# Optimization experiments

Hardware: AMD Instinct MI355X
Metric: run time of the kernel (lower is better)

The kernel has to match this reference:

```python
import jax, jax.numpy as jnp
import numpy as np

B, L, P = 16, 768, 256
EPS = 1e-6


def setup_inputs() -> dict:
    key = jax.random.key(0)
    k1, k2, k3, k4, k5 = jax.random.split(key, 5)
    pred = jax.random.normal(k1, (B, L, 3), dtype=jnp.float32) * 5.0
    target = pred + 0.5 * jax.random.normal(k2, (B, L, 3), dtype=jnp.float32)
    gen_mask = jax.random.randint(k3, (B, L), 0, 2).astype(jnp.int32)
    poc = jax.random.normal(k4, (B, P, 3), dtype=jnp.float32) * 5.0
    poc_mask = jax.random.randint(k5, (B, P), 0, 2).astype(jnp.int32)
    return {"pred": pred, "target": target, "gen_mask": gen_mask, "poc": poc, "poc_mask": poc_mask}


def _extract(fea, gm):
    # pad_sequence([fea[i][gm[i].bool()]]) equivalent, padded to L (extra zero
    # rows beyond the batch-max length are fully masked downstream, so losses
    # are identical to torch's pad-to-max behavior).
    order = jnp.argsort(jnp.where(gm > 0, 0, 1), axis=1)  # stable: valid rows first
    idx = order[..., None] if fea.ndim == 3 else order
    g = jnp.take_along_axis(fea, idx, axis=1)
    keep = jnp.arange(fea.shape[1])[None, :] < gm.sum(axis=1)[:, None]
    k = keep[..., None] if fea.ndim == 3 else keep
    return g * k.astype(fea.dtype)


def _masked_mean(t, m):
    # t: [B, L', 2]  m: [B, L']
    valid = jnp.clip(m.sum(axis=-1), 1e-6, None)
    return jnp.mean((t * m[..., None]).sum(axis=(-1, -2)) / valid)


def _cdist(a, b):
    # Gram-trick pairwise distances; [B, La, Lb] only (no [B,La,Lb,3] blowup).
    sq = (jnp.sum(a * a, -1)[:, :, None] + jnp.sum(b * b, -1)[:, None, :]
          - 2.0 * jnp.einsum('bid,bjd->bij', a, b))
    return jnp.sqrt(jnp.maximum(sq, 1e-12))


def _ca_angles(c):
    v1 = c[:, :-2] - c[:, 1:-1]
    v2 = c[:, 2:] - c[:, 1:-1]
    cos = jnp.sum(v1 * v2, -1) / (jnp.linalg.norm(v1, axis=-1) * jnp.linalg.norm(v2, axis=-1) + EPS)
    return jnp.arccos(jnp.clip(cos, -1.0, 1.0))


def _dihedrals(c):
    p0, p1, p2, p3 = c[:, :-3], c[:, 1:-2], c[:, 2:-1], c[:, 3:]
    v1, v2, v3 = p1 - p0, p2 - p1, p3 - p2
    n1 = jnp.cross(v1, v2)
    n2 = jnp.cross(v2, v3)
    cos = jnp.sum(n1 * n2, -1) / (jnp.linalg.norm(n1, axis=-1) * jnp.linalg.norm(n2, axis=-1) + EPS)
    phi = jnp.arccos(jnp.clip(cos, -1.0, 1.0))
    sign = jnp.sign(jnp.sum(jnp.cross(n1, n2) * v2, -1))
    return sign * phi


def _sincos(a):
    return jnp.stack([jnp.sin(a), jnp.cos(a)], axis=-1)


def _loss(pred, target, gen_mask, poc, poc_mask):
    gm = gen_mask.astype(jnp.float32)
    pred_e = _extract(pred, gen_mask)
    target_e = _extract(target, gen_mask)
    mask = _extract(gm, gen_mask)

    angle_loss = _masked_mean((_sincos(_ca_angles(pred_e)) - _sincos(_ca_angles(target_e))) ** 2,
                              mask[:, 1:-1])
    torsion_loss = _masked_mean((_sincos(_dihedrals(pred_e)) - _sincos(_dihedrals(target_e))) ** 2,
                                mask[:, 2:-1])

    d1 = _cdist(pred_e, pred_e)
    d2 = _cdist(target_e, target_e)
    dmask = mask[:, :, None] * mask[:, None, :]
    denom = jnp.sum(dmask, axis=(-1, -2)) + 1e-8
    dist_loss = jnp.mean(jnp.sum((d1 - d2) ** 2 * dmask, axis=(-1, -2)) / denom)
    clash = jnp.where((d1 < 3.8) & (d1 > 2.0), (3.8 - d1) ** 2, 0.0)
    clash_loss = jnp.mean(jnp.sum(clash * dmask, axis=(-1, -2)) / denom)

    # poc branch: source computes inter distances but then overwrites with
    # mean(dist_loss); replicated faithfully (inter_dist_loss == dist_loss).
    _ = _cdist(pred_e, poc)
    _ = _cdist(target_e, poc)
    inter_dist_loss = dist_loss

    return jnp.stack([angle_loss, torsion_loss, dist_loss, inter_dist_loss, clash_loss])


def reference(pred, target, gen_mask, poc, poc_mask):
    return _loss(pred, target, gen_mask, poc, poc_mask)
```

## Files before the change

### kernel.cpp

```cpp
#include <hip/hip_runtime.h>
#include <math.h>

#define BATCH 16
#define LSEQ 768
#define NCHUNK 16
#define NBLK (NCHUNK*BATCH)
#define NT 768
#define NWAVE (NT/64)


__device__ inline void angle_sc4(const float4* __restrict__ c, int i, float& s, float& co) {
    float4 a = c[i], b = c[i+1], d = c[i+2];
    float v1x = a.x-b.x, v1y = a.y-b.y, v1z = a.z-b.z;
    float v2x = d.x-b.x, v2y = d.y-b.y, v2z = d.z-b.z;
    float dot = v1x*v2x + v1y*v2y + v1z*v2z;
    float n1 = sqrtf(v1x*v1x + v1y*v1y + v1z*v1z);
    float n2 = sqrtf(v2x*v2x + v2y*v2y + v2z*v2z);
    float cv = dot / (n1*n2 + 1e-6f);
    cv = fminf(1.f, fmaxf(-1.f, cv));
    co = cv;
    s  = sqrtf(fmaxf(0.f, 1.f - cv*cv));
}

__device__ inline void dih_sc4(const float4* __restrict__ c, int i, float& s, float& co) {
    float4 p0 = c[i], p1 = c[i+1], p2 = c[i+2], p3 = c[i+3];
    float v1x = p1.x-p0.x, v1y = p1.y-p0.y, v1z = p1.z-p0.z;
    float v2x = p2.x-p1.x, v2y = p2.y-p1.y, v2z = p2.z-p1.z;
    float v3x = p3.x-p2.x, v3y = p3.y-p2.y, v3z = p3.z-p2.z;
    float n1x = v1y*v2z - v1z*v2y, n1y = v1z*v2x - v1x*v2z, n1z = v1x*v2y - v1y*v2x;
    float n2x = v2y*v3z - v2z*v3y, n2y = v2z*v3x - v2x*v3z, n2z = v2x*v3y - v2y*v3x;
    float dot = n1x*n2x + n1y*n2y + n1z*n2z;
    float l1 = sqrtf(n1x*n1x + n1y*n1y + n1z*n1z);
    float l2 = sqrtf(n2x*n2x + n2y*n2y + n2z*n2z);
    float cv = dot / (l1*l2 + 1e-6f);
    cv = fminf(1.f, fmaxf(-1.f, cv));
    float sinp = sqrtf(fmaxf(0.f, 1.f - cv*cv));
    float cx = n1y*n2z - n1z*n2y, cy = n1z*n2x - n1x*n2z, cz = n1x*n2y - n1y*n2x;
    float sg = cx*v2x + cy*v2y + cz*v2z;
    float sgn = (sg > 0.f) ? 1.f : ((sg < 0.f) ? -1.f : 0.f);
    co = cv;
    s  = sgn * sinp;
}


__global__ __launch_bounds__(NT) void k_main(
    const float* __restrict__ pred, const float* __restrict__ targ,
    const int* __restrict__ gm, float4* __restrict__ parts)
{
    const int b = blockIdx.y;
    const int c = blockIdx.x;
    const int t = threadIdx.x;
    const int lane = t & 63;
    const int wid = t >> 6;

    __shared__ float4 sp[LSEQ];
    __shared__ float4 st[LSEQ];
    __shared__ int   wtot[NWAVE];
    __shared__ float wred[NWAVE][4];

    const int m = gm[b*LSEQ + t];
    int inc = m;
    #pragma unroll
    for (int off = 1; off < 64; off <<= 1) {
        int v = __shfl_up(inc, off);
        if (lane >= off) inc += v;
    }
    if (lane == 63) wtot[wid] = inc;
    __syncthreads();
    int woff = 0, n = 0;
    #pragma unroll
    for (int w = 0; w < NWAVE; ++w) { int v = wtot[w]; n += v; if (w < wid) woff += v; }
    const int d = woff + inc - m;

    {
        int j = n + t;
        if (j < LSEQ) {
            sp[j] = make_float4(0.f, 0.f, 0.f, 0.f);
            st[j] = make_float4(0.f, 0.f, 0.f, 0.f);
        }
    }
    if (m) {
        const float* pb = pred + (b*LSEQ + t)*3;
        const float* tb = targ + (b*LSEQ + t)*3;
        float x = pb[0], y = pb[1], z = pb[2];
        sp[d] = make_float4(x, y, z, x*x + y*y + z*z);
        x = tb[0]; y = tb[1]; z = tb[2];
        st[d] = make_float4(x, y, z, x*x + y*y + z*z);
    }
    __syncthreads();

    float dist = 0.f, clash = 0.f;
    for (int r = c; r < n; r += NCHUNK) {
        const int j = r + 1 + t;
        if (j < n) {
            const float4 ai = sp[r];
            const float4 bi = st[r];
            float4 aj = sp[j];
            float4 bj = st[j];
            float sq1 = fmaxf(ai.w + aj.w - 2.f*(ai.x*aj.x + ai.y*aj.y + ai.z*aj.z), 1e-12f);
            float d1  = sqrtf(sq1);
            float sq2 = fmaxf(bi.w + bj.w - 2.f*(bi.x*bj.x + bi.y*bj.y + bi.z*bj.z), 1e-12f);
            float d2  = sqrtf(sq2);
            float dd = d1 - d2;
            dist += dd*dd;
            if (d1 < 3.8f && d1 > 2.0f) { float cv = 3.8f - d1; clash += cv*cv; }
        }
    }

    float aacc = 0.f, tacc = 0.f;
    if (t < LSEQ/NCHUNK) {
        const int i = c + NCHUNK*t;
        if (i < LSEQ-2 && i + 1 < n) {
            float s1, c1, s2, c2;
            angle_sc4(sp, i, s1, c1);
            angle_sc4(st, i, s2, c2);
            float ds = s1 - s2, dc = c1 - c2;
            aacc = ds*ds + dc*dc;
        }
        if (i < LSEQ-3 && i + 2 < n) {
            float s1, c1, s2, c2;
            dih_sc4(sp, i, s1, c1);
            dih_sc4(st, i, s2, c2);
            float ds = s1 - s2, dc = c1 - c2;
            tacc = ds*ds + dc*dc;
        }
    }

    #pragma unroll
    for (int off = 32; off; off >>= 1) {
        dist  += __shfl_down(dist,  off);
        clash += __shfl_down(clash, off);
        aacc  += __shfl_down(aacc,  off);
        tacc  += __shfl_down(tacc,  off);
    }
    if (lane == 0) { wred[wid][0]=dist; wred[wid][1]=clash; wred[wid][2]=aacc; wred[wid][3]=tacc; }
    __syncthreads();
    if (t == 0) {
        float ds = 0.f, cs = 0.f, as = 0.f, ts = 0.f;
        #pragma unroll
        for (int w = 0; w < NWAVE; ++w) { ds += wred[w][0]; cs += wred[w][1]; as += wred[w][2]; ts += wred[w][3]; }
        float denom = (float)n * (float)n + 1e-8f;
        int cai = n - 1; if (cai < 0) cai = 0; if (cai > LSEQ-2) cai = LSEQ-2;
        int cti = n - 2; if (cti < 0) cti = 0; if (cti > LSEQ-3) cti = LSEQ-3;
        parts[b*NCHUNK + c] = make_float4(2.f*ds/denom, 2.f*cs/denom,
                                          as / fmaxf((float)cai, 1e-6f),
                                          ts / fmaxf((float)cti, 1e-6f));
    }
}


__global__ __launch_bounds__(256) void k_final(
    const float4* __restrict__ parts, float* __restrict__ out)
{
    const int t = threadIdx.x;
    const int lane = t & 63;
    const int wid = t >> 6;
    __shared__ float wred[4][4];

    float4 p = parts[t];
    float fd = p.x, fc = p.y, fa = p.z, ft = p.w;
    #pragma unroll
    for (int off = 32; off; off >>= 1) {
        fd += __shfl_down(fd, off);
        fc += __shfl_down(fc, off);
        fa += __shfl_down(fa, off);
        ft += __shfl_down(ft, off);
    }
    if (lane == 0) { wred[wid][0]=fd; wred[wid][1]=fc; wred[wid][2]=fa; wred[wid][3]=ft; }
    __syncthreads();
    if (t == 0) {
        float d_ = 0.f, c_ = 0.f, a_ = 0.f, t_ = 0.f;
        #pragma unroll
        for (int w = 0; w < 4; ++w) { d_ += wred[w][0]; c_ += wred[w][1]; a_ += wred[w][2]; t_ += wred[w][3]; }
        out[0] = a_ / (float)BATCH;
        out[1] = t_ / (float)BATCH;
        out[2] = d_ / (float)BATCH;
        out[3] = d_ / (float)BATCH;
        out[4] = c_ / (float)BATCH;
    }
}

extern "C" void kernel_launch(void* const* d_in, const int* in_sizes, int n_in,
                              void* d_out, int out_size, void* d_ws, size_t ws_size,
                              hipStream_t stream) {
    (void)in_sizes; (void)n_in; (void)out_size; (void)ws_size;
    const float* pred = (const float*)d_in[0];
    const float* targ = (const float*)d_in[1];
    const int*   gm   = (const int*)d_in[2];

    float4* parts = (float4*)d_ws;
    float*  out   = (float*)d_out;

    k_main<<<dim3(NCHUNK, BATCH), NT, 0, stream>>>(pred, targ, gm, parts);
    k_final<<<1, 256, 0, stream>>>(parts, out);
}
```

Baseline: 15.49 us.

## Fuse final reduction into main kernel via per-block release/acquire flags

Drops the second reduction kernel. Each block now publishes its partial result and sets a magic flag with a release store, and block 0 spins with acquire loads until all 256 flags are set, then does the final reduction and clears the flags. This removes one kernel launch and its gap. In exchange it relies on every block being co-resident or scheduled ahead of block 0's wait, and on the workspace flags not already holding the magic value from stale memory.

```diff
diff --git a/kernel.cpp b/kernel.cpp
--- a/kernel.cpp
+++ b/kernel.cpp
@@ -7,6 +7,7 @@
 #define NBLK (NCHUNK*BATCH)
 #define NT 768
 #define NWAVE (NT/64)
+#define MAGIC 0x7F3A9C51DEADBEEFull
 
 
 __device__ inline void angle_sc4(const float4* __restrict__ c, int i, float& s, float& co) {
@@ -43,12 +44,14 @@
 }
 
 
-__global__ __launch_bounds__(NT) void k_main(
+__global__ __launch_bounds__(NT) void k_fused(
     const float* __restrict__ pred, const float* __restrict__ targ,
-    const int* __restrict__ gm, float4* __restrict__ parts)
+    const int* __restrict__ gm, float4* __restrict__ parts,
+    unsigned long long* __restrict__ flags, float* __restrict__ out)
 {
     const int b = blockIdx.y;
     const int c = blockIdx.x;
+    const int bid = b*NCHUNK + c;
     const int t = threadIdx.x;
     const int lane = t & 63;
     const int wid = t >> 6;
@@ -142,23 +145,28 @@
         float denom = (float)n * (float)n + 1e-8f;
         int cai = n - 1; if (cai < 0) cai = 0; if (cai > LSEQ-2) cai = LSEQ-2;
         int cti = n - 2; if (cti < 0) cti = 0; if (cti > LSEQ-3) cti = LSEQ-3;
-        parts[b*NCHUNK + c] = make_float4(2.f*ds/denom, 2.f*cs/denom,
-                                          as / fmaxf((float)cai, 1e-6f),
-                                          ts / fmaxf((float)cti, 1e-6f));
-    }
-}
-
-
-__global__ __launch_bounds__(256) void k_final(
-    const float4* __restrict__ parts, float* __restrict__ out)
-{
-    const int t = threadIdx.x;
-    const int lane = t & 63;
-    const int wid = t >> 6;
-    __shared__ float wred[4][4];
-
-    float4 p = parts[t];
-    float fd = p.x, fc = p.y, fa = p.z, ft = p.w;
+        parts[bid] = make_float4(2.f*ds/denom, 2.f*cs/denom,
+                                 as / fmaxf((float)cai, 1e-6f),
+                                 ts / fmaxf((float)cti, 1e-6f));
+        __hip_atomic_store(&flags[bid], MAGIC, __ATOMIC_RELEASE,
+                           __HIP_MEMORY_SCOPE_AGENT);
+    }
+
+    if (bid != 0) return;
+
+    if (t < NBLK) {
+        while (__hip_atomic_load(&flags[t], __ATOMIC_ACQUIRE,
+                                 __HIP_MEMORY_SCOPE_AGENT) != MAGIC) {
+            __builtin_amdgcn_s_sleep(1);
+        }
+    }
+    __syncthreads();
+
+    float fd = 0.f, fc = 0.f, fa = 0.f, ft = 0.f;
+    if (t < NBLK) {
+        float4 p = parts[t];
+        fd = p.x; fc = p.y; fa = p.z; ft = p.w;
+    }
     #pragma unroll
     for (int off = 32; off; off >>= 1) {
         fd += __shfl_down(fd, off);
@@ -171,12 +179,17 @@
     if (t == 0) {
         float d_ = 0.f, c_ = 0.f, a_ = 0.f, t_ = 0.f;
         #pragma unroll
-        for (int w = 0; w < 4; ++w) { d_ += wred[w][0]; c_ += wred[w][1]; a_ += wred[w][2]; t_ += wred[w][3]; }
+        for (int w = 0; w < NWAVE; ++w) { d_ += wred[w][0]; c_ += wred[w][1]; a_ += wred[w][2]; t_ += wred[w][3]; }
         out[0] = a_ / (float)BATCH;
         out[1] = t_ / (float)BATCH;
         out[2] = d_ / (float)BATCH;
         out[3] = d_ / (float)BATCH;
         out[4] = c_ / (float)BATCH;
+    }
+
+    if (t < NBLK) {
+        __hip_atomic_store(&flags[t], 0ull, __ATOMIC_RELAXED,
+                           __HIP_MEMORY_SCOPE_AGENT);
     }
 }
 
@@ -188,9 +201,9 @@
     const float* targ = (const float*)d_in[1];
     const int*   gm   = (const int*)d_in[2];
 
-    float4* parts = (float4*)d_ws;
-    float*  out   = (float*)d_out;
-
-    k_main<<<dim3(NCHUNK, BATCH), NT, 0, stream>>>(pred, targ, gm, parts);
-    k_final<<<1, 256, 0, stream>>>(parts, out);
-}
+    float4*             parts = (float4*)d_ws;
+    unsigned long long* flags = (unsigned long long*)(parts + NBLK);
+    float*              out   = (float*)d_out;
+
+    k_fused<<<dim3(NCHUNK, BATCH), NT, 0, stream>>>(pred, targ, gm, parts, flags, out);
+}
```

Result: slower. 17.66 us (+14.0%).
